# Kernel tuning notes

Measured on AMD Instinct MI355X. Metric: run time of the kernel, lower is better.

Reference implementation:

```python
import jax, jax.numpy as jnp
import numpy as np
import math

B, D, OUT = 512, 128, 100000
S, M = 32.0, 0.5
COS_M, SIN_M = math.cos(M), math.sin(M)
TH = math.cos(math.pi - M)
MM = math.sin(math.pi - M) * M
M1 = M2 = M3 = M5 = 1.0


def setup_inputs() -> dict:
    key = jax.random.key(0)
    k1, k2, k3, k4, k5, k6 = jax.random.split(key, 6)
    x = jax.random.normal(k1, (B, D), dtype=jnp.float32)
    label = jax.random.randint(k2, (B,), 0, OUT)
    k = jax.random.uniform(k3, (1, 1, 1024, 1024), dtype=jnp.float32)
    x0 = jax.random.uniform(k4, (1, 3, 112, 96), dtype=jnp.float32)
    img = jax.random.uniform(k5, (1, 3, 112, 96), dtype=jnp.float32)
    # xavier_uniform for [OUT, D]
    limit = math.sqrt(6.0 / (OUT + D))
    W = jax.random.uniform(k6, (OUT, D), minval=-limit, maxval=limit, dtype=jnp.float32)
    return {"x": x, "label": label, "k": k, "x0": x0, "img": img, "W": W}


def _arcmargin(x, W, label):
    xn = x / jnp.linalg.norm(x, axis=-1, keepdims=True)
    wn = W / jnp.linalg.norm(W, axis=-1, keepdims=True)
    cosine = xn @ wn.T                                  # [B, OUT]
    sine = jnp.sqrt(jnp.clip(1.0 - cosine * cosine, 0.0))
    phi = cosine * COS_M - sine * SIN_M
    phi = jnp.where(cosine - TH > 0, phi, cosine - MM)   # easy_margin=False
    one_hot = jax.nn.one_hot(label, OUT, dtype=cosine.dtype)
    logits = S * (one_hot * phi + (1.0 - one_hot) * cosine)
    logp = jax.nn.log_softmax(logits, axis=-1)
    return -jnp.mean(jnp.take_along_axis(logp, label[:, None], axis=1))


def _tv_loss(k):
    h, w = k.shape[-2], k.shape[-1]
    count_h = (h - 1) * w
    count_w = h * (w - 1)
    h_tv = jnp.sum((k[:, :, 1:, :] - k[:, :, :-1, :]) ** 2)
    w_tv = jnp.sum((k[:, :, :, 1:] - k[:, :, :, :-1]) ** 2)
    return -1.0 * 2.0 * (h_tv / count_h + w_tv / count_w)  # weight = -1*loss_weight


def _bin_loss(k):
    # sum over pixels of k^2 + (k-1)^2, / (h*w), then mean over batch/channel
    return jnp.mean(k * k + (k - 1.0) ** 2)


def _inv_loss(k):
    k = jax.lax.stop_gradient(k)  # original detaches before numpy FFT
    mag = jnp.abs(jnp.fft.fftn(k, axes=(-2, -1)))
    return jnp.mean(jnp.sum(mag, axis=(-1, -2)))  # L1 norm over (-1,-2), then mean


def reference(x, label, k, x0, img, W):
    loss = (M1 * _arcmargin(x, W, label)
            + M2 * _tv_loss(k)
            + M3 * _bin_loss(k)
            + M5 * _inv_loss(k))
    return loss
```

## Files before the change

### kernel.cpp

```cpp
#include <hip/hip_runtime.h>


typedef float f32x4 __attribute__((ext_vector_type(4)));
typedef unsigned short u16;
typedef unsigned int u32;
typedef unsigned long long u64;

#define BATCH 512
#define DIM 128
#define OUTN 100000
#define NOBLK 782
#define NROW2 1564
#define CHUNKS 16
#define CHSZ2 98
#define SSCALE 32.0f
#define K2C 46.166241308446828f
#define COSM 0.8775825618903728f
#define SINM 0.479425538604203f
#define THC (-0.8775825618903728f)
#define MMC 0.2397127693021015f

#define S1_FFT 1024
#define S1_XP  1152
#define S1_NW  13664

#define S2_GEMM0 256
#define S2_TV0   3392
#define S2_NBLK  4416

#define DEC8(v, j) __builtin_amdgcn_cvt_f32_fp8((int)(v), (j))

__device__ inline float waveRedSum(float v) {
#pragma unroll
  for (int off = 1; off < 64; off <<= 1) v += __shfl_xor(v, off, 64);
  return v;
}

__device__ inline float halfRedSum(float v) {
#pragma unroll
  for (int off = 1; off < 32; off <<= 1) v += __shfl_xor(v, off, 64);
  return v;
}

__global__ __launch_bounds__(256) void stage1_k(const float* __restrict__ x,
                                                const float* __restrict__ W,
                                                const int* __restrict__ label,
                                                const float* __restrict__ kimg,
                                                char* __restrict__ xh8,
                                                float* __restrict__ coslab,
                                                char* __restrict__ Wh8,
                                                float2* __restrict__ fbuf) {
  __shared__ __align__(16) char smem[12288];
  int t = threadIdx.x;
  int bid = blockIdx.x;

  if (bid < S1_FFT) {
    float2* tw = (float2*)smem;
    float2* arr = (float2*)(smem + 4096);
    int r = bid;
#pragma unroll
    for (int i = 0; i < 2; i++) {
      int j = i * 256 + t;
      float s, c;
      __sincosf(-0.006135923151542565f * (float)j, &s, &c);
      tw[j] = make_float2(c, s);
    }
#pragma unroll
    for (int i = 0; i < 4; i++) {
      int idx = i * 256 + t;
      arr[idx] = make_float2(kimg[r * 1024 + idx], 0.f);
    }
    __syncthreads();
    for (int lh = 9; lh >= 0; lh--) {
      int hlf = 1 << lh;
#pragma unroll
      for (int i = 0; i < 2; i++) {
        int bf = i * 256 + t;
        int pos = bf & (hlf - 1);
        int g = bf >> lh;
        int i0 = (g << (lh + 1)) + pos;
        int i1 = i0 + hlf;
        float2 u = arr[i0], v = arr[i1];
        float2 w = tw[pos << (9 - lh)];
        arr[i0] = make_float2(u.x + v.x, u.y + v.y);
        float dr = u.x - v.x, di = u.y - v.y;
        arr[i1] = make_float2(dr * w.x - di * w.y, dr * w.y + di * w.x);
      }
      __syncthreads();
    }
#pragma unroll
    for (int i = 0; i < 4; i++) {
      int idx = i * 256 + t;
      fbuf[(size_t)r * 1024 + idx] = arr[idx];
    }
  } else if (bid < S1_XP) {
    int b = (bid - S1_FFT) * 4 + (t >> 6);
    int lane = t & 63;
    size_t xb = (size_t)b * DIM;
    float2 v = *(const float2*)&x[xb + lane * 2];
    int lab = label[b];
    size_t wb = (size_t)lab * DIM;
    float2 w = *(const float2*)&W[wb + lane * 2];
    float ss = waveRedSum(v.x * v.x + v.y * v.y);
    float d  = waveRedSum(v.x * w.x + v.y * w.y);
    float nw = waveRedSum(w.x * w.x + w.y * w.y);
    float inv = rsqrtf(ss);
    u32 pk = __builtin_amdgcn_cvt_pk_fp8_f32(v.x * inv, v.y * inv, 0, 0);
    *(u16*)&xh8[b * 128 + lane * 2] = (u16)pk;
    if (lane == 0) coslab[b] = d * rsqrtf(ss * nw);
  } else {
    int p = (bid - S1_XP) * 4 + (t >> 6);
    int lane = t & 63;
    int r = 2 * p + (lane >> 5);
    int col = (lane & 31) * 4;
    if (2 * p >= OUTN) {
      *(u32*)&Wh8[(size_t)r * 128 + col] = 0u;
      return;
    }
    float4 v = *(const float4*)&W[(size_t)r * DIM + col];
    float ss = halfRedSum(v.x * v.x + v.y * v.y + v.z * v.z + v.w * v.w);
    float inv = rsqrtf(ss);
    u32 pk = __builtin_amdgcn_cvt_pk_fp8_f32(v.x * inv, v.y * inv, 0, 0);
    pk = __builtin_amdgcn_cvt_pk_fp8_f32(v.z * inv, v.w * inv, pk, 1);
    *(u32*)&Wh8[(size_t)r * 128 + col] = pk;
  }
}

__global__ __launch_bounds__(256, 4) void stage2_k(const char* __restrict__ Wh8,
                                                   const char* __restrict__ xh8,
                                                   float* __restrict__ gpart,
                                                   const float2* __restrict__ fbuf,
                                                   float* __restrict__ fftpart,
                                                   const float* __restrict__ kimg,
                                                   float4* __restrict__ tvpart) {
  __shared__ __align__(16) char smem[36880];
  int t = threadIdx.x;
  int bid = blockIdx.x;

  if (bid >= S2_TV0) {
    int r = bid - S2_TV0;
    int idx = r * 1024 + t * 4;
    float4 v = *(const float4*)&kimg[idx];
    float bs = v.x * v.x + (v.x - 1.f) * (v.x - 1.f)
             + v.y * v.y + (v.y - 1.f) * (v.y - 1.f)
             + v.z * v.z + (v.z - 1.f) * (v.z - 1.f)
             + v.w * v.w + (v.w - 1.f) * (v.w - 1.f);
    float d0 = v.y - v.x, d1 = v.z - v.y, d2 = v.w - v.z;
    float wsm = d0 * d0 + d1 * d1 + d2 * d2;
    if (t < 255) { float e4 = kimg[idx + 4]; float d3 = e4 - v.w; wsm += d3 * d3; }
    float hs = 0.f;
    if (r < 1023) {
      float4 n = *(const float4*)&kimg[idx + 1024];
      float h0 = n.x - v.x, h1 = n.y - v.y, h2 = n.z - v.z, h3 = n.w - v.w;
      hs = h0 * h0 + h1 * h1 + h2 * h2 + h3 * h3;
    }
    hs = waveRedSum(hs); wsm = waveRedSum(wsm); bs = waveRedSum(bs);
    float (*red)[4] = (float(*)[4])smem;
    if ((t & 63) == 0) { int w = t >> 6; red[0][w] = hs; red[1][w] = wsm; red[2][w] = bs; }
    __syncthreads();
    if (t == 0)
      tvpart[r] = make_float4(red[0][0] + red[0][1] + red[0][2] + red[0][3],
                              red[1][0] + red[1][1] + red[1][2] + red[1][3],
                              red[2][0] + red[2][1] + red[2][2] + red[2][3], 0.f);
  } else if (bid >= S2_GEMM0) {
    int wgrp = (bid - S2_GEMM0) & 31, g = (bid - S2_GEMM0) >> 5;
    int o = g * 8 + (wgrp & 7), bt = wgrp >> 3;
    if (o >= NOBLK) return;
    int o0 = o * 128, b0 = bt * 128;
    char* Ash = smem;
    char* Bsh = smem + 16384;
    int wv = t >> 6, lane = t & 63;
    int wo = (wv & 1) << 6, wbs = (wv >> 1) << 6;
    int m16 = lane & 15, q = lane >> 4;

    int r8 = t >> 3, cB = (t & 7) * 16, c0 = (t & 7) * 2;
#pragma unroll
    for (int it = 0; it < 4; it++) {
      int r = it * 32 + r8;
      int s = r & 15;
      uint4 va = *(const uint4*)&Wh8[(size_t)(o0 + r) * 128 + cB];
      *(u64*)&Ash[r * 128 + ((c0 ^ s) << 3)]       = ((u64)va.y << 32) | va.x;
      *(u64*)&Ash[r * 128 + (((c0 + 1) ^ s) << 3)] = ((u64)va.w << 32) | va.z;
      uint4 vb = *(const uint4*)&xh8[(size_t)(b0 + r) * 128 + cB];
      *(u64*)&Bsh[r * 128 + ((c0 ^ s) << 3)]       = ((u64)vb.y << 32) | vb.x;
      *(u64*)&Bsh[r * 128 + (((c0 + 1) ^ s) << 3)] = ((u64)vb.w << 32) | vb.z;
    }
    __syncthreads();

    f32x4 acc[4][4] = {};
#pragma unroll
    for (int kk = 0; kk < 4; kk++) {
      long af[4], bf[4];
#pragma unroll
      for (int i = 0; i < 4; i++) {
        int row = wo + i * 16 + m16;
        af[i] = *(const long*)&Ash[row * 128 + (((kk * 4 + q) ^ (row & 15)) << 3)];
      }
#pragma unroll
      for (int j = 0; j < 4; j++) {
        int row = wbs + j * 16 + m16;
        bf[j] = *(const long*)&Bsh[row * 128 + (((kk * 4 + q) ^ (row & 15)) << 3)];
      }
#pragma unroll
      for (int i = 0; i < 4; i++)
#pragma unroll
        for (int j = 0; j < 4; j++)
          acc[i][j] = __builtin_amdgcn_mfma_f32_16x16x32_fp8_fp8(af[i], bf[j], acc[i][j], 0, 0, 0);
    }
#pragma unroll
    for (int j = 0; j < 4; j++) {
      float s = 0.f;
#pragma unroll
      for (int i = 0; i < 4; i++)
#pragma unroll
        for (int r = 0; r < 4; r++)
          s += exp2f(K2C * acc[i][j][r]);
      s += __shfl_xor(s, 16, 64);
      s += __shfl_xor(s, 32, 64);
      if (q == 0)
        gpart[(size_t)(o * 2 + (wv & 1)) * 512 + b0 + wbs + j * 16 + m16] = s;
    }
  } else {
    float2* arr = (float2*)smem;
    float2* tw = (float2*)(smem + 32768);
    float* red = (float*)(smem + 36864);
    int c0 = bid * 4;
#pragma unroll
    for (int i = 0; i < 2; i++) {
      int j = i * 256 + t;
      float s, c;
      __sincosf(-0.006135923151542565f * (float)j, &s, &c);
      tw[j] = make_float2(c, s);
    }
#pragma unroll
    for (int i = 0; i < 16; i++) {
      int li = i * 256 + t;
      int rr = li >> 2, c = li & 3;
      arr[rr * 4 + c] = fbuf[(size_t)rr * 1024 + c0 + c];
    }
    __syncthreads();
    for (int lh = 9; lh >= 0; lh--) {
      int hlf = 1 << lh;
#pragma unroll
      for (int i = 0; i < 8; i++) {
        int w = i * 256 + t;
        int c = w & 3, bf = w >> 2;
        int pos = bf & (hlf - 1), g2i = bf >> lh;
        int i0 = ((g2i << (lh + 1)) + pos) * 4 + c;
        int i1 = i0 + hlf * 4;
        float2 u = arr[i0], v = arr[i1];
        float2 tww = tw[pos << (9 - lh)];
        arr[i0] = make_float2(u.x + v.x, u.y + v.y);
        float dr = u.x - v.x, di = u.y - v.y;
        arr[i1] = make_float2(dr * tww.x - di * tww.y, dr * tww.y + di * tww.x);
      }
      __syncthreads();
    }
    float s = 0.f;
#pragma unroll
    for (int i = 0; i < 16; i++) {
      float2 v = arr[i * 256 + t];
      s += sqrtf(v.x * v.x + v.y * v.y);
    }
    s = waveRedSum(s);
    if ((t & 63) == 0) red[t >> 6] = s;
    __syncthreads();
    if (t == 0) fftpart[bid] = red[0] + red[1] + red[2] + red[3];
  }
}

__global__ __launch_bounds__(256) void gemmred_k(const float* __restrict__ gpart,
                                                 float* __restrict__ g2,
                                                 const char* __restrict__ xh8,
                                                 const char* __restrict__ Wh8,
                                                 const int* __restrict__ label,
                                                 float* __restrict__ labexp) {
  int t = threadIdx.x;
  int blk = blockIdx.x;
  if (blk < 32) {
    int chunk = blk >> 1, half = blk & 1;
    int b = half * 256 + t;
    int rBeg = chunk * CHSZ2;
    int rEnd = rBeg + CHSZ2; if (rEnd > NROW2) rEnd = NROW2;
    float s = 0.f;
    for (int r = rBeg; r < rEnd; r++) s += gpart[(size_t)r * 512 + b];
    g2[chunk * 512 + b] = s;
  } else {
    int b = (blk - 32) * 256 + t;
    int lab = label[b];
    const u32* xr = (const u32*)(xh8 + (size_t)b * 128);
    const u32* wr = (const u32*)(Wh8 + (size_t)lab * 128);
    float d = 0.f;
#pragma unroll 4
    for (int i = 0; i < 32; i++) {
      u32 xa = xr[i], wa = wr[i];
      d += DEC8(xa, 0) * DEC8(wa, 0) + DEC8(xa, 1) * DEC8(wa, 1)
         + DEC8(xa, 2) * DEC8(wa, 2) + DEC8(xa, 3) * DEC8(wa, 3);
    }
    labexp[b] = exp2f(K2C * d);
  }
}

__global__ __launch_bounds__(256) void final_k(const float* __restrict__ coslab,
                                               const float* __restrict__ g2,
                                               const float4* __restrict__ tvpart,
                                               const float* __restrict__ fftpart,
                                               const float* __restrict__ labexp,
                                               float* __restrict__ out) {
  int t = threadIdx.x;
  float arc = 0.f, hs = 0.f, wsm = 0.f, bs = 0.f, fs = 0.f;
#pragma unroll
  for (int i = 0; i < 2; i++) {
    int b = i * 256 + t;
    float se = 0.f;
#pragma unroll
    for (int c = 0; c < CHUNKS; c++) se += g2[c * 512 + b];
    se -= 96.0f;
    se -= labexp[b];
    float cl = coslab[b];
    float sine = sqrtf(fmaxf(0.f, 1.f - cl * cl));
    float phi = cl * COSM - sine * SINM;
    if (!(cl - THC > 0.f)) phi = cl - MMC;
    arc += __logf(se + exp2f(K2C * phi)) - SSCALE * phi;
  }
#pragma unroll
  for (int i = 0; i < 4; i++) {
    float4 p = tvpart[i * 256 + t];
    hs += p.x; wsm += p.y; bs += p.z;
  }
  fs = fftpart[t];
  arc = waveRedSum(arc); hs = waveRedSum(hs); wsm = waveRedSum(wsm);
  bs = waveRedSum(bs); fs = waveRedSum(fs);
  __shared__ float red[5][4];
  if ((t & 63) == 0) {
    int w = t >> 6;
    red[0][w] = arc; red[1][w] = hs; red[2][w] = wsm; red[3][w] = bs; red[4][w] = fs;
  }
  __syncthreads();
  if (t == 0) {
    float A = 0, H = 0, Wv = 0, Bv = 0, F = 0;
#pragma unroll
    for (int w = 0; w < 4; w++) {
      A += red[0][w]; H += red[1][w]; Wv += red[2][w]; Bv += red[3][w]; F += red[4][w];
    }
    float cnt = 1023.0f * 1024.0f;
    out[0] = A * (1.0f / 512.0f) - 2.0f * (H / cnt + Wv / cnt)
           + Bv * (1.0f / 1048576.0f) + F;
  }
}

extern "C" void kernel_launch(void* const* d_in, const int* in_sizes, int n_in,
                              void* d_out, int out_size, void* d_ws, size_t ws_size,
                              hipStream_t stream) {
  const float* x = (const float*)d_in[0];
  const int* label = (const int*)d_in[1];
  const float* kimg = (const float*)d_in[2];
  const float* W = (const float*)d_in[5];
  float* out = (float*)d_out;
  char* ws = (char*)d_ws;
  float*  coslab  = (float*)(ws + 0);
  char*   xh8     = (char*)(ws + 2048);
  char*   Wh8     = (char*)(ws + 67584);
  float2* fbuf    = (float2*)(ws + 12879872);
  float*  gpart   = (float*)(ws + 21268480);
  float*  g2      = (float*)(ws + 24471552);
  float4* tvpart  = (float4*)(ws + 24504320);
  float*  fftpart = (float*)(ws + 24520704);
  float*  labexp  = (float*)(ws + 24521728);

  hipLaunchKernelGGL(stage1_k, dim3(S1_NW), dim3(256), 0, stream,
                     x, W, label, kimg, xh8, coslab, Wh8, fbuf);
  hipLaunchKernelGGL(stage2_k, dim3(S2_NBLK), dim3(256), 0, stream,
                     Wh8, xh8, gpart, fbuf, fftpart, kimg, tvpart);
  hipLaunchKernelGGL(gemmred_k, dim3(34), dim3(256), 0, stream,
                     gpart, g2, xh8, Wh8, label, labexp);
  hipLaunchKernelGGL(final_k, dim3(1), dim3(256), 0, stream,
                     coslab, g2, tvpart, fftpart, labexp, out);
}
```

Baseline: 154.6 us.

## Pack real FFT rows in pairs, halve column FFTs, fuse final reduction

The row FFT now packs two real rows into one complex FFT and splits them using Hermitian symmetry. Only 516 columns (513 useful) are stored, so about half as many column FFT blocks run, and the magnitude sum weights interior columns by two. The separate final kernel is removed: the last block of gemmred, picked with an atomic counter and thread fences, does the final reduction. This saves a launch and about half the FFT work, at the cost of atomic and fence overhead and a counter reset done inside stage1.

```diff
diff --git a/kernel.cpp b/kernel.cpp
--- a/kernel.cpp
+++ b/kernel.cpp
@@ -13,6 +13,7 @@
 #define NROW2 1564
 #define CHUNKS 16
 #define CHSZ2 98
+#define NCOL 516
 #define SSCALE 32.0f
 #define K2C 46.166241308446828f
 #define COSM 0.8775825618903728f
@@ -20,13 +21,13 @@
 #define THC (-0.8775825618903728f)
 #define MMC 0.2397127693021015f
 
-#define S1_FFT 1024
-#define S1_XP  1152
-#define S1_NW  13664
-
-#define S2_GEMM0 256
-#define S2_TV0   3392
-#define S2_NBLK  4416
+#define S1_FFT 512
+#define S1_XP  640
+#define S1_NW  13152
+
+#define S2_GEMM0 129
+#define S2_TV0   3265
+#define S2_NBLK  4289
 
 #define DEC8(v, j) __builtin_amdgcn_cvt_f32_fp8((int)(v), (j))
 
@@ -49,7 +50,8 @@
                                                 char* __restrict__ xh8,
                                                 float* __restrict__ coslab,
                                                 char* __restrict__ Wh8,
-                                                float2* __restrict__ fbuf) {
+                                                float2* __restrict__ fbuf,
+                                                int* __restrict__ cnt) {
   __shared__ __align__(16) char smem[12288];
   int t = threadIdx.x;
   int bid = blockIdx.x;
@@ -68,7 +70,7 @@
 #pragma unroll
     for (int i = 0; i < 4; i++) {
       int idx = i * 256 + t;
-      arr[idx] = make_float2(kimg[r * 1024 + idx], 0.f);
+      arr[idx] = make_float2(kimg[(2 * r) * 1024 + idx], kimg[(2 * r + 1) * 1024 + idx]);
     }
     __syncthreads();
     for (int lh = 9; lh >= 0; lh--) {
@@ -89,11 +91,24 @@
       __syncthreads();
     }
 #pragma unroll
-    for (int i = 0; i < 4; i++) {
-      int idx = i * 256 + t;
-      fbuf[(size_t)r * 1024 + idx] = arr[idx];
+    for (int it = 0; it < 3; it++) {
+      int k = it * 256 + t;
+      if (k < NCOL) {
+        float2 fa = make_float2(0.f, 0.f), fb = make_float2(0.f, 0.f);
+        if (k < 513) {
+          int j1 = __brev((u32)k) >> 22;
+          int j2 = __brev((u32)((1024 - k) & 1023)) >> 22;
+          float2 z1 = arr[j1], z2 = arr[j2];
+          fa = make_float2(0.5f * (z1.x + z2.x), 0.5f * (z1.y - z2.y));
+          float uu = z1.x - z2.x, vv = z1.y + z2.y;
+          fb = make_float2(0.5f * vv, -0.5f * uu);
+        }
+        fbuf[(size_t)(2 * r) * NCOL + k] = fa;
+        fbuf[(size_t)(2 * r + 1) * NCOL + k] = fb;
+      }
     }
   } else if (bid < S1_XP) {
+    if (bid == S1_FFT && t == 0) *cnt = 0;
     int b = (bid - S1_FFT) * 4 + (t >> 6);
     int lane = t & 63;
     size_t xb = (size_t)b * DIM;
@@ -236,7 +251,7 @@
     for (int i = 0; i < 16; i++) {
       int li = i * 256 + t;
       int rr = li >> 2, c = li & 3;
-      arr[rr * 4 + c] = fbuf[(size_t)rr * 1024 + c0 + c];
+      arr[rr * 4 + c] = fbuf[(size_t)rr * NCOL + c0 + c];
     }
     __syncthreads();
     for (int lh = 9; lh >= 0; lh--) {
@@ -259,8 +274,11 @@
     float s = 0.f;
 #pragma unroll
     for (int i = 0; i < 16; i++) {
-      float2 v = arr[i * 256 + t];
-      s += sqrtf(v.x * v.x + v.y * v.y);
+      int li = i * 256 + t;
+      int col = c0 + (li & 3);
+      float w = (col == 0 || col == 512) ? 1.f : (col < 512 ? 2.f : 0.f);
+      float2 v = arr[li];
+      s += w * sqrtf(v.x * v.x + v.y * v.y);
     }
     s = waveRedSum(s);
     if ((t & 63) == 0) red[t >> 6] = s;
@@ -274,7 +292,12 @@
                                                  const char* __restrict__ xh8,
                                                  const char* __restrict__ Wh8,
                                                  const int* __restrict__ label,
-                                                 float* __restrict__ labexp) {
+                                                 float* __restrict__ labexp,
+                                                 const float* __restrict__ coslab,
+                                                 const float4* __restrict__ tvpart,
+                                                 const float* __restrict__ fftpart,
+                                                 int* __restrict__ cnt,
+                                                 float* __restrict__ out) {
   int t = threadIdx.x;
   int blk = blockIdx.x;
   if (blk < 32) {
@@ -299,15 +322,15 @@
     }
     labexp[b] = exp2f(K2C * d);
   }
-}
-
-__global__ __launch_bounds__(256) void final_k(const float* __restrict__ coslab,
-                                               const float* __restrict__ g2,
-                                               const float4* __restrict__ tvpart,
-                                               const float* __restrict__ fftpart,
-                                               const float* __restrict__ labexp,
-                                               float* __restrict__ out) {
-  int t = threadIdx.x;
+
+  __shared__ int lastFlag;
+  __threadfence();
+  __syncthreads();
+  if (t == 0) lastFlag = (atomicAdd(cnt, 1) == 33);
+  __syncthreads();
+  if (!lastFlag) return;
+  __threadfence();
+
   float arc = 0.f, hs = 0.f, wsm = 0.f, bs = 0.f, fs = 0.f;
 #pragma unroll
   for (int i = 0; i < 2; i++) {
@@ -328,7 +351,7 @@
     float4 p = tvpart[i * 256 + t];
     hs += p.x; wsm += p.y; bs += p.z;
   }
-  fs = fftpart[t];
+  fs = (t < S2_GEMM0) ? fftpart[t] : 0.f;
   arc = waveRedSum(arc); hs = waveRedSum(hs); wsm = waveRedSum(wsm);
   bs = waveRedSum(bs); fs = waveRedSum(fs);
   __shared__ float red[5][4];
@@ -343,8 +366,8 @@
     for (int w = 0; w < 4; w++) {
       A += red[0][w]; H += red[1][w]; Wv += red[2][w]; Bv += red[3][w]; F += red[4][w];
     }
-    float cnt = 1023.0f * 1024.0f;
-    out[0] = A * (1.0f / 512.0f) - 2.0f * (H / cnt + Wv / cnt)
+    float cnt2 = 1023.0f * 1024.0f;
+    out[0] = A * (1.0f / 512.0f) - 2.0f * (H / cnt2 + Wv / cnt2)
            + Bv * (1.0f / 1048576.0f) + F;
   }
 }
@@ -362,18 +385,18 @@
   char*   xh8     = (char*)(ws + 2048);
   char*   Wh8     = (char*)(ws + 67584);
   float2* fbuf    = (float2*)(ws + 12879872);
-  float*  gpart   = (float*)(ws + 21268480);
-  float*  g2      = (float*)(ws + 24471552);
-  float4* tvpart  = (float4*)(ws + 24504320);
-  float*  fftpart = (float*)(ws + 24520704);
-  float*  labexp  = (float*)(ws + 24521728);
+  float*  gpart   = (float*)(ws + 17106944);
+  float*  g2      = (float*)(ws + 20310016);
+  float4* tvpart  = (float4*)(ws + 20342784);
+  float*  fftpart = (float*)(ws + 20359168);
+  float*  labexp  = (float*)(ws + 20361216);
+  int*    cnt     = (int*)(ws + 20363264);
 
   hipLaunchKernelGGL(stage1_k, dim3(S1_NW), dim3(256), 0, stream,
-                     x, W, label, kimg, xh8, coslab, Wh8, fbuf);
+                     x, W, label, kimg, xh8, coslab, Wh8, fbuf, cnt);
   hipLaunchKernelGGL(stage2_k, dim3(S2_NBLK), dim3(256), 0, stream,
                      Wh8, xh8, gpart, fbuf, fftpart, kimg, tvpart);
   hipLaunchKernelGGL(gemmred_k, dim3(34), dim3(256), 0, stream,
-                     gpart, g2, xh8, Wh8, label, labexp);
-  hipLaunchKernelGGL(final_k, dim3(1), dim3(256), 0, stream,
-                     coslab, g2, tvpart, fftpart, labexp, out);
-}
+                     gpart, g2, xh8, Wh8, label, labexp,
+                     coslab, tvpart, fftpart, cnt, out);
+}
```

After: 151.2 us. -2.2%, faster.
